# Performance work log

Hardware: AMD Instinct MI355X
Metric: run time of the kernel (lower is better)

## Reference

```python
import jax, jax.numpy as jnp
import numpy as np

B, T, E, H, D = 4, 2048, 1024, 16, 64


def setup_inputs() -> dict:
    key = jax.random.key(0)
    k1, k2, k3, k4 = jax.random.split(key, 4)
    s = 1.0 / np.sqrt(E)
    return {
        "x": jax.random.normal(k1, (B, T, E), dtype=jnp.float32),
        "wj_w": jax.random.uniform(k2, (E, E), jnp.float32, -s, s),   # torch Linear weight (out,in)
        "wjv_w": jax.random.uniform(k3, (E, E), jnp.float32, -s, s),
        "wo_w": jax.random.uniform(k4, (E, H * D), jnp.float32, -s, s),
    }


def reference(x, wj_w, wjv_w, wo_w):
    b, t, e = x.shape
    # echo = x @ wj_w.T ; eb = echo @ wj_w  (F.linear with transposed weight)
    eb = (x @ wj_w.T) @ wj_w
    sc = jnp.sum(x * eb, axis=-1) / jnp.sqrt(jnp.asarray(e, x.dtype))  # (B,T)
    # rank-1 outer-product scores with strict-upper causal mask
    ja = sc[:, :, None] * sc[:, None, :]                               # (B,T,T)
    causal = jnp.tril(jnp.ones((t, t), dtype=bool))
    ja = jnp.where(causal[None], ja, -jnp.inf)
    ja = jax.nn.softmax(ja, axis=-1)                                   # (B,T,T)
    # values per head; attention map shared across heads (broadcast, not materialized)
    val = (x @ wjv_w.T).reshape(b, t, H, D)                            # (B,T,H,D)
    out = jnp.einsum("bts,bshd->bthd", ja, val)                       # (B,T,H,D)
    return out.reshape(b, t, H * D) @ wo_w.T                           # (B,T,E)
```

## Files before the change

### kernel.cpp

```cpp
#include <hip/hip_runtime.h>
#include <math.h>

#define R_ROWS 8192
#define T_SEQ  2048
#define E_DIM  1024
#define KC     32

typedef __attribute__((ext_vector_type(8))) short short8;
typedef __attribute__((ext_vector_type(4))) float f32x4;

__device__ __forceinline__ ushort f2bf(float f) {
  uint u = __float_as_uint(f);
  u += 0x7FFFu + ((u >> 16) & 1u);
  return (ushort)(u >> 16);
}
__device__ __forceinline__ float bf2f(ushort h) {
  return __uint_as_float(((uint)h) << 16);
}


__global__ __launch_bounds__(256) void cvt_split_frag(
    const float* __restrict__ in, ushort* __restrict__ hi,
    ushort* __restrict__ lo, int n)
{
  int g = blockIdx.x * 256 + threadIdx.x;
  if (g >= n) return;
  const int l = g & 15, h = (g >> 4) & 3;
  const int pq = g >> 6;
  const int q = pq & (KC - 1), p = pq >> 5;
  const size_t src = (size_t)(p * 16 + l) * 1024 + q * 32 + h * 8;
  const float4 v0 = *(const float4*)&in[src];
  const float4 v1 = *(const float4*)&in[src + 4];
  ushort hh[8], ll[8];
  const float v[8] = {v0.x, v0.y, v0.z, v0.w, v1.x, v1.y, v1.z, v1.w};
#pragma unroll
  for (int e = 0; e < 8; ++e) {
    hh[e] = f2bf(v[e]);
    ll[e] = f2bf(v[e] - bf2f(hh[e]));
  }
  *(uint4*)&hi[(size_t)g * 8] = *(const uint4*)hh;
  *(uint4*)&lo[(size_t)g * 8] = *(const uint4*)ll;
}

__global__ __launch_bounds__(256) void cvt_bf16_frag(
    const float* __restrict__ in, ushort* __restrict__ out, int n)
{
  int g = blockIdx.x * 256 + threadIdx.x;
  if (g >= n) return;
  const int l = g & 15, h = (g >> 4) & 3;
  const int pq = g >> 6;
  const int q = pq & (KC - 1), p = pq >> 5;
  const size_t src = (size_t)(p * 16 + l) * 1024 + q * 32 + h * 8;
  const float4 v0 = *(const float4*)&in[src];
  const float4 v1 = *(const float4*)&in[src + 4];
  ushort hh[8];
  const float v[8] = {v0.x, v0.y, v0.z, v0.w, v1.x, v1.y, v1.z, v1.w};
#pragma unroll
  for (int e = 0; e < 8; ++e) hh[e] = f2bf(v[e]);
  *(uint4*)&out[(size_t)g * 8] = *(const uint4*)hh;
}

__global__ __launch_bounds__(256) void cvt_bf16(
    const float* __restrict__ in, ushort* __restrict__ out, int n4)
{
  int i = blockIdx.x * 256 + threadIdx.x;
  if (i >= n4) return;
  float4 v = ((const float4*)in)[i];
  ushort4 o;
  o.x = f2bf(v.x); o.y = f2bf(v.y); o.z = f2bf(v.z); o.w = f2bf(v.w);
  ((ushort4*)out)[i] = o;
}

struct Frags { short8 ah[4], al[4], bh[4], bl[4]; };

__global__ __launch_bounds__(256, 2) void gemm_sq_direct(
    const ushort* __restrict__ xh, const ushort* __restrict__ xl,
    const ushort* __restrict__ wh, const ushort* __restrict__ wl,
    float* __restrict__ sc_raw)
{
  const int tid = threadIdx.x;
  const int m0 = blockIdx.y * 128, n0 = blockIdx.x * 128;
  const int wave = tid >> 6, lane = tid & 63;
  const int l15 = lane & 15, lq = lane >> 4;
  const int wm = (wave & 1) * 64, wn = (wave >> 1) * 64;

  size_t aoff[4], boff[4];
#pragma unroll
  for (int i = 0; i < 4; ++i)
    aoff[i] = ((size_t)(((m0 + wm) >> 4) + i) * KC * 4 + lq) * 128 + l15 * 8;
#pragma unroll
  for (int j = 0; j < 4; ++j)
    boff[j] = ((size_t)(((n0 + wn) >> 4) + j) * KC * 4 + lq) * 128 + l15 * 8;

  f32x4 acc[4][4] = {};
  Frags f0, f1;

  auto load = [&](Frags& f, int q) {
    const size_t dq = (size_t)q * 512;
#pragma unroll
    for (int i = 0; i < 4; ++i) {
      f.ah[i] = *(const short8*)(xh + aoff[i] + dq);
      f.al[i] = *(const short8*)(xl + aoff[i] + dq);
    }
#pragma unroll
    for (int j = 0; j < 4; ++j) {
      f.bh[j] = *(const short8*)(wh + boff[j] + dq);
      f.bl[j] = *(const short8*)(wl + boff[j] + dq);
    }
  };
  auto step = [&](const Frags& f) {
#pragma unroll
    for (int i = 0; i < 4; ++i)
#pragma unroll
      for (int j = 0; j < 4; ++j) {
        acc[i][j] = __builtin_amdgcn_mfma_f32_16x16x32_bf16(f.ah[i], f.bh[j], acc[i][j], 0, 0, 0);
        acc[i][j] = __builtin_amdgcn_mfma_f32_16x16x32_bf16(f.ah[i], f.bl[j], acc[i][j], 0, 0, 0);
        acc[i][j] = __builtin_amdgcn_mfma_f32_16x16x32_bf16(f.al[i], f.bh[j], acc[i][j], 0, 0, 0);
      }
  };

  load(f0, 0);
#pragma unroll 1
  for (int q = 0; q < KC; q += 2) {
    load(f1, q + 1);
    step(f0);
    if (q + 2 < KC) load(f0, q + 2);
    step(f1);
  }

  __shared__ float red[128][33];
#pragma unroll
  for (int i = 0; i < 4; ++i)
#pragma unroll
    for (int r = 0; r < 4; ++r) {
      const int row = wm + i * 16 + lq * 4 + r;
      float s = 0.f;
#pragma unroll
      for (int j = 0; j < 4; ++j) s += acc[i][j][r] * acc[i][j][r];
      red[row][(l15 << 1) | (wave >> 1)] = s;
    }
  __syncthreads();
  if (tid < 128) {
    float s = 0.f;
#pragma unroll
    for (int c = 0; c < 32; ++c) s += red[tid][c];
    atomicAdd(&sc_raw[m0 + tid], s);
  }
}

__global__ __launch_bounds__(1024) void scan_max(
    const float* __restrict__ sc_raw, float* __restrict__ sc,
    float* __restrict__ pmax)
{
  const int b = blockIdx.x;
  __shared__ float b0[T_SEQ];
  __shared__ float b1[T_SEQ];
  const int tid = threadIdx.x;
  for (int i = tid; i < T_SEQ; i += 1024) {
    const float v = sc_raw[b*T_SEQ + i] * 0.03125f;
    b0[i] = v;
    sc[b*T_SEQ + i] = v;
  }
  __syncthreads();
  float* src = b0; float* dst = b1;
  for (int off = 1; off < T_SEQ; off <<= 1) {
    for (int i = tid; i < T_SEQ; i += 1024)
      dst[i] = (i >= off) ? fmaxf(src[i], src[i - off]) : src[i];
    __syncthreads();
    float* tmp = src; src = dst; dst = tmp;
  }
  for (int i = tid; i < T_SEQ; i += 1024) pmax[b*T_SEQ + i] = src[i];
}

template<bool OUT_BF16>
__global__ __launch_bounds__(256) void gemm_bf16_bfrag(
    const ushort* __restrict__ A, const ushort* __restrict__ Bf,
    void* __restrict__ Cout, int N, int K)
{
  __shared__ ushort As[128][40];
  const int tid = threadIdx.x;
  const int m0 = blockIdx.y * 128, n0 = blockIdx.x * 128;
  const int wave = tid >> 6, lane = tid & 63;
  const int l15 = lane & 15, lq = lane >> 4;
  const int wm = (wave & 1) * 64, wn = (wave >> 1) * 64;
  const int srow = tid >> 2, scol = (tid & 3) * 8;
  const int Kc = K >> 5;

  f32x4 acc[4][4] = {};
  const ushort* Ap = A + (size_t)(m0 + srow) * K + scol;
  size_t boff[4];
#pragma unroll
  for (int j = 0; j < 4; ++j)
    boff[j] = ((size_t)(((n0 + wn) >> 4) + j) * Kc * 4 + lq) * 128 + l15 * 8;

  for (int q = 0; q < Kc; ++q) {
    const uint4 a0 = *(const uint4*)(Ap + q * 32);
    const uint4 a1 = *(const uint4*)(Ap + (size_t)64 * K + q * 32);
    short8 bfr[4];
#pragma unroll
    for (int j = 0; j < 4; ++j)
      bfr[j] = *(const short8*)(Bf + boff[j] + (size_t)q * 512);
    __syncthreads();
    *(uint4*)&As[srow     ][scol] = a0;
    *(uint4*)&As[srow + 64][scol] = a1;
    __syncthreads();
    short8 af[4];
#pragma unroll
    for (int i = 0; i < 4; ++i)
      af[i] = *(const short8*)&As[wm + i*16 + l15][lq*8];
#pragma unroll
    for (int i = 0; i < 4; ++i)
#pragma unroll
      for (int j = 0; j < 4; ++j)
        acc[i][j] = __builtin_amdgcn_mfma_f32_16x16x32_bf16(af[i], bfr[j], acc[i][j], 0, 0, 0);
  }

#pragma unroll
  for (int i = 0; i < 4; ++i)
#pragma unroll
    for (int j = 0; j < 4; ++j) {
      const int mb = m0 + wm + i*16 + lq*4;
      const int nb = n0 + wn + j*16 + l15;
#pragma unroll
      for (int r = 0; r < 4; ++r) {
        if (OUT_BF16)
          ((ushort*)Cout)[(size_t)(mb + r) * N + nb] = f2bf(acc[i][j][r]);
        else
          ((float*)Cout)[(size_t)(mb + r) * N + nb] = acc[i][j][r];
      }
    }
}

__global__ __launch_bounds__(512) void attn_mfma(
    const ushort* __restrict__ valT, const float* __restrict__ sc,
    const float* __restrict__ pmax, ushort* __restrict__ attnN)
{
  __shared__ float scs_all[T_SEQ];
  __shared__ ushort p[2][128][72];
  __shared__ float zsh[128][4];
  __shared__ float zinv[128];

  const int b  = blockIdx.z;
  const int e0 = blockIdx.x * 128;
  const int tid = threadIdx.x;
  const int wave = tid >> 6, lane = tid & 63;
  const int l15 = lane & 15, lq = lane >> 4;
  const int wm = (wave & 1) * 64;
  const int wn = (wave >> 1) * 32;
  const int bT = b * T_SEQ;

  *(float4*)&scs_all[tid * 4] = *(const float4*)&sc[bT + tid * 4];
  __syncthreads();

  const int prow = tid >> 2;
  const int pc = (tid & 3) * 16;

#pragma unroll 1
  for (int ph = 0; ph < 2; ++ph) {
    const int ty = ph == 0 ? (15 - (int)blockIdx.y) : (int)blockIdx.y;
    const int t0 = ty * 128;
    const int nchunk = 2 * ty + 2;

    const int tglob = t0 + prow;
    const float st = sc[bT + tglob];
    const float pm = pmax[bT + tglob];

    f32x4 acc[4][2] = {};
    float zp = 0.f;

    auto pgen = [&](int c, int buf) -> float {
      const int s0 = c * 64;
      float sv[16];
#pragma unroll
      for (int q = 0; q < 4; ++q)
        *(float4*)&sv[q*4] = *(const float4*)&scs_all[s0 + pc + q*4];
      ushort tmp[16];
      float z = 0.f;
#pragma unroll
      for (int k = 0; k < 16; ++k) {
        const int sg = s0 + pc + k;
        float pe = 0.f;
        if (sg <= tglob) pe = __expf(st * (sv[k] - pm));
        const ushort h = f2bf(pe);
        tmp[k] = h;
        z += bf2f(h);
      }
      *(uint4*)&p[buf][prow][pc    ] = *(const uint4*)&tmp[0];
      *(uint4*)&p[buf][prow][pc + 8] = *(const uint4*)&tmp[8];
      return z;
    };

    auto loadB = [&](short8* dst, int c) {
#pragma unroll
      for (int j = 0; j < 2; ++j)
#pragma unroll
        for (int ksi = 0; ksi < 2; ++ksi)
          dst[j*2 + ksi] = *(const short8*)&valT[
              (size_t)(e0 + wn + j*16 + l15) * R_ROWS + bT + c*64 + ksi*32 + lq*8];
    };

    auto mstep = [&](int buf, const short8* bfr) {
#pragma unroll
      for (int ksi = 0; ksi < 2; ++ksi) {
        short8 af[4];
#pragma unroll
        for (int i = 0; i < 4; ++i)
          af[i] = *(const short8*)&p[buf][wm + i*16 + l15][ksi*32 + lq*8];
#pragma unroll
        for (int i = 0; i < 4; ++i)
#pragma unroll
          for (int j = 0; j < 2; ++j)
            acc[i][j] = __builtin_amdgcn_mfma_f32_16x16x32_bf16(
                af[i], bfr[j*2 + ksi], acc[i][j], 0, 0, 0);
      }
    };

    short8 bA[4], bB[4];
    zp += pgen(0, 0);
    loadB(bA, 0);
    __syncthreads();

#pragma unroll 1
    for (int c = 0; c < nchunk; ++c) {
      if ((c & 1) == 0) {
        if (c + 1 < nchunk) { loadB(bB, c + 1); zp += pgen(c + 1, 1); }
        mstep(0, bA);
      } else {
        if (c + 1 < nchunk) { loadB(bA, c + 1); zp += pgen(c + 1, 0); }
        mstep(1, bB);
      }
      __syncthreads();
    }

    zsh[prow][tid & 3] = zp;
    __syncthreads();
    if (tid < 128)
      zinv[tid] = 1.0f / (zsh[tid][0] + zsh[tid][1] + zsh[tid][2] + zsh[tid][3]);
    __syncthreads();

#pragma unroll
    for (int i = 0; i < 4; ++i)
#pragma unroll
      for (int j = 0; j < 2; ++j) {
        const int nb = e0 + wn + j*16 + l15;
#pragma unroll
        for (int r = 0; r < 4; ++r) {
          const int ml = wm + i*16 + lq*4 + r;
          const float v = acc[i][j][r] * zinv[ml];
          attnN[(size_t)(bT + t0 + ml) * E_DIM + nb] = f2bf(v);
        }
      }
    __syncthreads();
  }
}

extern "C" void kernel_launch(void* const* d_in, const int* in_sizes, int n_in,
                              void* d_out, int out_size, void* d_ws, size_t ws_size,
                              hipStream_t stream) {
  (void)in_sizes; (void)n_in; (void)out_size; (void)ws_size;
  const float* x   = (const float*)d_in[0];
  const float* wj  = (const float*)d_in[1];
  const float* wjv = (const float*)d_in[2];
  const float* wo  = (const float*)d_in[3];
  float* out = (float*)d_out;

  ushort* xh_f  = (ushort*)d_ws;
  ushort* xl_f  = xh_f  + (size_t)R_ROWS * E_DIM;
  ushort* wjh_f = xl_f  + (size_t)R_ROWS * E_DIM;
  ushort* wjl_f = wjh_f + (size_t)E_DIM * E_DIM;
  ushort* wjvb  = wjl_f + (size_t)E_DIM * E_DIM;
  ushort* wob_f = wjvb  + (size_t)E_DIM * E_DIM;
  float* sc_raw = (float*)(wob_f + (size_t)E_DIM * E_DIM);
  float* sc     = sc_raw + R_ROWS;
  float* pmax   = sc + R_ROWS;
  ushort* valT  = xl_f;
  ushort* attnN = xh_f;

  hipMemsetAsync(sc_raw, 0, R_ROWS * sizeof(float), stream);

  cvt_split_frag<<<R_ROWS*E_DIM/8/256, 256, 0, stream>>>(x,  xh_f,  xl_f,  R_ROWS*E_DIM/8);
  cvt_split_frag<<<E_DIM*E_DIM/8/256, 256, 0, stream>>>(wj, wjh_f, wjl_f, E_DIM*E_DIM/8);
  cvt_bf16<<<E_DIM*E_DIM/4/256, 256, 0, stream>>>(wjv, wjvb, E_DIM*E_DIM/4);
  cvt_bf16_frag<<<E_DIM*E_DIM/8/256, 256, 0, stream>>>(wo, wob_f, E_DIM*E_DIM/8);

  gemm_sq_direct<<<dim3(E_DIM/128, R_ROWS/128), 256, 0, stream>>>(
      xh_f, xl_f, wjh_f, wjl_f, sc_raw);
  scan_max<<<4, 1024, 0, stream>>>(sc_raw, sc, pmax);

  gemm_bf16_bfrag<true><<<dim3(R_ROWS/128, E_DIM/128), 256, 0, stream>>>(
      wjvb, xh_f, valT, R_ROWS, E_DIM);

  attn_mfma<<<dim3(E_DIM/128, 8, 4), 512, 0, stream>>>(valT, sc, pmax, attnN);

  gemm_bf16_bfrag<false><<<dim3(E_DIM/128, R_ROWS/128), 256, 0, stream>>>(
      attnN, wob_f, out, E_DIM, E_DIM);
}
```

Before: 271.8 us.

## Split attention into P-generation kernel and fragment-layout MFMA GEMM

The causal softmax probability tiles are now computed once per batch in a separate kernel and stored to workspace in MFMA fragment order, with row sums accumulated atomically into a Z buffer. The attention GEMM reads P fragments and values straight from global memory into registers with double buffering and no LDS or barriers, and uses a 64x64 per-wave tile. Previously each of the 8 column blocks recomputed the exponentials. The cost is an extra launch, global traffic for the P tiles, and a reworked workspace layout that reuses the wj buffers once they are consumed.

```diff
diff --git a/kernel.cpp b/kernel.cpp
--- a/kernel.cpp
+++ b/kernel.cpp
@@ -172,6 +172,142 @@
   for (int i = tid; i < T_SEQ; i += 1024) pmax[b*T_SEQ + i] = src[i];
 }
 
+__global__ __launch_bounds__(256) void pgen(
+    const float* __restrict__ sc, const float* __restrict__ pmax,
+    ushort* __restrict__ Pfrag, float* __restrict__ Z)
+{
+  const int b = blockIdx.y;
+  const int cb = blockIdx.x;
+  int ty = (int)((sqrtf(4.0f * cb + 1.0f) - 1.0f) * 0.5f);
+  while ((ty + 1) * (ty + 2) <= cb) ++ty;
+  while (ty * (ty + 1) > cb) --ty;
+  const int c = cb - ty * (ty + 1);
+  const int t0 = ty * 128, s0 = c * 64;
+  const int bT = b * T_SEQ;
+  const int tid = threadIdx.x;
+
+  __shared__ float stv[128], pmv[128], scs[64], zacc[128];
+  if (tid < 128) {
+    stv[tid] = sc[bT + t0 + tid];
+    pmv[tid] = pmax[bT + t0 + tid];
+    zacc[tid] = 0.f;
+  } else if (tid < 192) {
+    scs[tid - 128] = sc[bT + s0 + (tid - 128)];
+  }
+  __syncthreads();
+
+  ushort* base = Pfrag + (size_t)(b * 272 + cb) * 8192;
+#pragma unroll
+  for (int i = 0; i < 4; ++i) {
+    const int run = tid * 4 + i;
+    const int r  = ((run >> 7) << 4) | (run & 15);
+    const int sb = (((run >> 6) & 1) << 5) | (((run >> 4) & 3) << 3);
+    const float st = stv[r], pm = pmv[r];
+    const int tg = t0 + r, sg0 = s0 + sb;
+    ushort tmp[8];
+    float z = 0.f;
+#pragma unroll
+    for (int k = 0; k < 8; ++k) {
+      float pe = 0.f;
+      if (sg0 + k <= tg) pe = __expf(st * (scs[sb + k] - pm));
+      const ushort hb = f2bf(pe);
+      tmp[k] = hb;
+      z += bf2f(hb);
+    }
+    *(uint4*)(base + run * 8) = *(const uint4*)tmp;
+    if (z != 0.f) atomicAdd(&zacc[r], z);
+  }
+  __syncthreads();
+  if (tid < 128 && zacc[tid] != 0.f)
+    atomicAdd(&Z[bT + t0 + tid], zacc[tid]);
+}
+
+__global__ __launch_bounds__(256, 2) void attn_gemm(
+    const ushort* __restrict__ Pfrag, const ushort* __restrict__ valT,
+    const float* __restrict__ Z, ushort* __restrict__ attnN)
+{
+  const int b = blockIdx.z;
+  const int e0 = blockIdx.x * 128;
+  const int tid = threadIdx.x;
+  const int wave = tid >> 6, lane = tid & 63;
+  const int l15 = lane & 15, lq = lane >> 4;
+  const int wm = (wave & 1) * 64, wn = (wave >> 1) * 64;
+  const int bT = b * T_SEQ;
+
+#pragma unroll 1
+  for (int ph = 0; ph < 2; ++ph) {
+    const int ty = ph ? (int)blockIdx.y : 15 - (int)blockIdx.y;
+    const int t0 = ty * 128;
+    const int nch = 2 * ty + 2;
+    const ushort* pb = Pfrag + (size_t)(b * 272 + ty * (ty + 1)) * 8192;
+
+    size_t aoffs[4][2];
+#pragma unroll
+    for (int i = 0; i < 4; ++i)
+#pragma unroll
+      for (int ksi = 0; ksi < 2; ++ksi)
+        aoffs[i][ksi] =
+            (size_t)(((((wm >> 4) + i) * 2 + ksi) * 4 + lq) * 128 + l15 * 8);
+    const ushort* vbase = valT + bT + lq * 8;
+    size_t voffs[4];
+#pragma unroll
+    for (int j = 0; j < 4; ++j)
+      voffs[j] = (size_t)(e0 + wn + j * 16 + l15) * R_ROWS;
+
+    f32x4 acc[4][4] = {};
+    short8 a0[4][2], v0[4][2], a1[4][2], v1[4][2];
+
+    auto load = [&](short8 (&a)[4][2], short8 (&v)[4][2], int c) {
+      const ushort* cbp = pb + (size_t)c * 8192;
+      const ushort* vb = vbase + c * 64;
+#pragma unroll
+      for (int i = 0; i < 4; ++i) {
+        a[i][0] = *(const short8*)(cbp + aoffs[i][0]);
+        a[i][1] = *(const short8*)(cbp + aoffs[i][1]);
+      }
+#pragma unroll
+      for (int j = 0; j < 4; ++j) {
+        v[j][0] = *(const short8*)(vb + voffs[j]);
+        v[j][1] = *(const short8*)(vb + voffs[j] + 32);
+      }
+    };
+    auto step = [&](short8 (&a)[4][2], short8 (&v)[4][2]) {
+#pragma unroll
+      for (int ksi = 0; ksi < 2; ++ksi)
+#pragma unroll
+        for (int i = 0; i < 4; ++i)
+#pragma unroll
+          for (int j = 0; j < 4; ++j)
+            acc[i][j] = __builtin_amdgcn_mfma_f32_16x16x32_bf16(
+                a[i][ksi], v[j][ksi], acc[i][j], 0, 0, 0);
+    };
+
+    load(a0, v0, 0);
+#pragma unroll 1
+    for (int c = 0; c < nch; c += 2) {
+      load(a1, v1, c + 1);
+      step(a0, v0);
+      if (c + 2 < nch) load(a0, v0, c + 2);
+      step(a1, v1);
+    }
+
+#pragma unroll
+    for (int i = 0; i < 4; ++i) {
+      const int mlb = t0 + wm + i * 16 + lq * 4;
+      float zi[4];
+#pragma unroll
+      for (int r = 0; r < 4; ++r) zi[r] = 1.0f / Z[bT + mlb + r];
+#pragma unroll
+      for (int j = 0; j < 4; ++j) {
+        const int nb = e0 + wn + j * 16 + l15;
+#pragma unroll
+        for (int r = 0; r < 4; ++r)
+          attnN[(size_t)(bT + mlb + r) * E_DIM + nb] = f2bf(acc[i][j][r] * zi[r]);
+      }
+    }
+  }
+}
+
 template<bool OUT_BF16>
 __global__ __launch_bounds__(256) void gemm_bf16_bfrag(
     const ushort* __restrict__ A, const ushort* __restrict__ Bf,
@@ -229,129 +365,6 @@
           ((float*)Cout)[(size_t)(mb + r) * N + nb] = acc[i][j][r];
       }
     }
-}
-
-__global__ __launch_bounds__(512) void attn_mfma(
-    const ushort* __restrict__ valT, const float* __restrict__ sc,
-    const float* __restrict__ pmax, ushort* __restrict__ attnN)
-{
-  __shared__ float scs_all[T_SEQ];
-  __shared__ ushort p[2][128][72];
-  __shared__ float zsh[128][4];
-  __shared__ float zinv[128];
-
-  const int b  = blockIdx.z;
-  const int e0 = blockIdx.x * 128;
-  const int tid = threadIdx.x;
-  const int wave = tid >> 6, lane = tid & 63;
-  const int l15 = lane & 15, lq = lane >> 4;
-  const int wm = (wave & 1) * 64;
-  const int wn = (wave >> 1) * 32;
-  const int bT = b * T_SEQ;
-
-  *(float4*)&scs_all[tid * 4] = *(const float4*)&sc[bT + tid * 4];
-  __syncthreads();
-
-  const int prow = tid >> 2;
-  const int pc = (tid & 3) * 16;
-
-#pragma unroll 1
-  for (int ph = 0; ph < 2; ++ph) {
-    const int ty = ph == 0 ? (15 - (int)blockIdx.y) : (int)blockIdx.y;
-    const int t0 = ty * 128;
-    const int nchunk = 2 * ty + 2;
-
-    const int tglob = t0 + prow;
-    const float st = sc[bT + tglob];
-    const float pm = pmax[bT + tglob];
-
-    f32x4 acc[4][2] = {};
-    float zp = 0.f;
-
-    auto pgen = [&](int c, int buf) -> float {
-      const int s0 = c * 64;
-      float sv[16];
-#pragma unroll
-      for (int q = 0; q < 4; ++q)
-        *(float4*)&sv[q*4] = *(const float4*)&scs_all[s0 + pc + q*4];
-      ushort tmp[16];
-      float z = 0.f;
-#pragma unroll
-      for (int k = 0; k < 16; ++k) {
-        const int sg = s0 + pc + k;
-        float pe = 0.f;
-        if (sg <= tglob) pe = __expf(st * (sv[k] - pm));
-        const ushort h = f2bf(pe);
-        tmp[k] = h;
-        z += bf2f(h);
-      }
-      *(uint4*)&p[buf][prow][pc    ] = *(const uint4*)&tmp[0];
-      *(uint4*)&p[buf][prow][pc + 8] = *(const uint4*)&tmp[8];
-      return z;
-    };
-
-    auto loadB = [&](short8* dst, int c) {
-#pragma unroll
-      for (int j = 0; j < 2; ++j)
-#pragma unroll
-        for (int ksi = 0; ksi < 2; ++ksi)
-          dst[j*2 + ksi] = *(const short8*)&valT[
-              (size_t)(e0 + wn + j*16 + l15) * R_ROWS + bT + c*64 + ksi*32 + lq*8];
-    };
-
-    auto mstep = [&](int buf, const short8* bfr) {
-#pragma unroll
-      for (int ksi = 0; ksi < 2; ++ksi) {
-        short8 af[4];
-#pragma unroll
-        for (int i = 0; i < 4; ++i)
-          af[i] = *(const short8*)&p[buf][wm + i*16 + l15][ksi*32 + lq*8];
-#pragma unroll
-        for (int i = 0; i < 4; ++i)
-#pragma unroll
-          for (int j = 0; j < 2; ++j)
-            acc[i][j] = __builtin_amdgcn_mfma_f32_16x16x32_bf16(
-                af[i], bfr[j*2 + ksi], acc[i][j], 0, 0, 0);
-      }
-    };
-
-    short8 bA[4], bB[4];
-    zp += pgen(0, 0);
-    loadB(bA, 0);
-    __syncthreads();
-
-#pragma unroll 1
-    for (int c = 0; c < nchunk; ++c) {
-      if ((c & 1) == 0) {
-        if (c + 1 < nchunk) { loadB(bB, c + 1); zp += pgen(c + 1, 1); }
-        mstep(0, bA);
-      } else {
-        if (c + 1 < nchunk) { loadB(bA, c + 1); zp += pgen(c + 1, 0); }
-        mstep(1, bB);
-      }
-      __syncthreads();
-    }
-
-    zsh[prow][tid & 3] = zp;
-    __syncthreads();
-    if (tid < 128)
-      zinv[tid] = 1.0f / (zsh[tid][0] + zsh[tid][1] + zsh[tid][2] + zsh[tid][3]);
-    __syncthreads();
-
-#pragma unroll
-    for (int i = 0; i < 4; ++i)
-#pragma unroll
-      for (int j = 0; j < 2; ++j) {
-        const int nb = e0 + wn + j*16 + l15;
-#pragma unroll
-        for (int r = 0; r < 4; ++r) {
-          const int ml = wm + i*16 + lq*4 + r;
-          const float v = acc[i][j][r] * zinv[ml];
-          attnN[(size_t)(bT + t0 + ml) * E_DIM + nb] = f2bf(v);
-        }
-      }
-    __syncthreads();
-  }
 }
 
 extern "C" void kernel_launch(void* const* d_in, const int* in_sizes, int n_in,
@@ -368,15 +381,17 @@
   ushort* xl_f  = xh_f  + (size_t)R_ROWS * E_DIM;
   ushort* wjh_f = xl_f  + (size_t)R_ROWS * E_DIM;
   ushort* wjl_f = wjh_f + (size_t)E_DIM * E_DIM;
-  ushort* wjvb  = wjl_f + (size_t)E_DIM * E_DIM;
-  ushort* wob_f = wjvb  + (size_t)E_DIM * E_DIM;
-  float* sc_raw = (float*)(wob_f + (size_t)E_DIM * E_DIM);
-  float* sc     = sc_raw + R_ROWS;
+  ushort* Pfrag = wjh_f;
+  float* sc_raw = (float*)(Pfrag + (size_t)1088 * 8192);
+  float* Zbuf   = sc_raw + R_ROWS;
+  float* sc     = Zbuf + R_ROWS;
   float* pmax   = sc + R_ROWS;
+  ushort* wjvb  = (ushort*)(pmax + R_ROWS);
+  ushort* wob_f = wjvb + (size_t)E_DIM * E_DIM;
   ushort* valT  = xl_f;
   ushort* attnN = xh_f;
 
-  hipMemsetAsync(sc_raw, 0, R_ROWS * sizeof(float), stream);
+  hipMemsetAsync(sc_raw, 0, 2 * R_ROWS * sizeof(float), stream);
 
   cvt_split_frag<<<R_ROWS*E_DIM/8/256, 256, 0, stream>>>(x,  xh_f,  xl_f,  R_ROWS*E_DIM/8);
   cvt_split_frag<<<E_DIM*E_DIM/8/256, 256, 0, stream>>>(wj, wjh_f, wjl_f, E_DIM*E_DIM/8);
@@ -390,7 +405,9 @@
   gemm_bf16_bfrag<true><<<dim3(R_ROWS/128, E_DIM/128), 256, 0, stream>>>(
       wjvb, xh_f, valT, R_ROWS, E_DIM);
 
-  attn_mfma<<<dim3(E_DIM/128, 8, 4), 512, 0, stream>>>(valT, sc, pmax, attnN);
+  pgen<<<dim3(272, 4), 256, 0, stream>>>(sc, pmax, Pfrag, Zbuf);
+
+  attn_gemm<<<dim3(E_DIM/128, 8, 4), 256, 0, stream>>>(Pfrag, valT, Zbuf, attnN);
 
   gemm_bf16_bfrag<false><<<dim3(E_DIM/128, R_ROWS/128), 256, 0, stream>>>(
       attnN, wob_f, out, E_DIM, E_DIM);
```

After: 291.6 us. +7.3%, slower.

## Retile attention kernel to 64 query rows by 256 value columns with finer causal chunks

Applied to the files above, without the earlier changes.

Changes the attention tile from 128 query rows by 128 value columns to 64 rows by 256 columns, with each wave computing 32x64 instead of 64x32. Causal chunking now skips at 64-row granularity, which cuts the wasted masked work along the diagonal. The mask check is applied only on the last chunk, and the exponent argument is folded into a single fmaf. The cost is more B-fragment registers per wave and more blocks, while P generation per value column is amortized over twice as many columns.

```diff
diff --git a/kernel.cpp b/kernel.cpp
--- a/kernel.cpp
+++ b/kernel.cpp
@@ -236,63 +236,71 @@
     const float* __restrict__ pmax, ushort* __restrict__ attnN)
 {
   __shared__ float scs_all[T_SEQ];
-  __shared__ ushort p[2][128][72];
-  __shared__ float zsh[128][4];
-  __shared__ float zinv[128];
+  __shared__ ushort p[2][64][72];
+  __shared__ float zsh[64][9];
+  __shared__ float zinv[64];
 
   const int b  = blockIdx.z;
-  const int e0 = blockIdx.x * 128;
+  const int e0 = blockIdx.x * 256;
   const int tid = threadIdx.x;
   const int wave = tid >> 6, lane = tid & 63;
   const int l15 = lane & 15, lq = lane >> 4;
-  const int wm = (wave & 1) * 64;
-  const int wn = (wave >> 1) * 32;
+  const int wm = (wave & 1) * 32;
+  const int wn = (wave >> 1) * 64;
   const int bT = b * T_SEQ;
 
   *(float4*)&scs_all[tid * 4] = *(const float4*)&sc[bT + tid * 4];
   __syncthreads();
 
-  const int prow = tid >> 2;
-  const int pc = (tid & 3) * 16;
+  const int prow = tid >> 3;
+  const int pc = (tid & 7) * 8;
 
 #pragma unroll 1
   for (int ph = 0; ph < 2; ++ph) {
-    const int ty = ph == 0 ? (15 - (int)blockIdx.y) : (int)blockIdx.y;
-    const int t0 = ty * 128;
-    const int nchunk = 2 * ty + 2;
-
+    const int ty = ph ? (int)blockIdx.y : 31 - (int)blockIdx.y;
+    const int t0 = ty * 64;
+    const int nch = ty + 1;
+
+    const float st = scs_all[t0 + prow];
+    const float nd = -st * pmax[bT + t0 + prow];
     const int tglob = t0 + prow;
-    const float st = sc[bT + tglob];
-    const float pm = pmax[bT + tglob];
-
-    f32x4 acc[4][2] = {};
+
+    f32x4 acc[2][4] = {};
     float zp = 0.f;
 
     auto pgen = [&](int c, int buf) -> float {
       const int s0 = c * 64;
-      float sv[16];
-#pragma unroll
-      for (int q = 0; q < 4; ++q)
-        *(float4*)&sv[q*4] = *(const float4*)&scs_all[s0 + pc + q*4];
-      ushort tmp[16];
+      float sv[8];
+      *(float4*)&sv[0] = *(const float4*)&scs_all[s0 + pc];
+      *(float4*)&sv[4] = *(const float4*)&scs_all[s0 + pc + 4];
+      ushort tmp[8];
       float z = 0.f;
-#pragma unroll
-      for (int k = 0; k < 16; ++k) {
-        const int sg = s0 + pc + k;
-        float pe = 0.f;
-        if (sg <= tglob) pe = __expf(st * (sv[k] - pm));
-        const ushort h = f2bf(pe);
-        tmp[k] = h;
-        z += bf2f(h);
-      }
-      *(uint4*)&p[buf][prow][pc    ] = *(const uint4*)&tmp[0];
-      *(uint4*)&p[buf][prow][pc + 8] = *(const uint4*)&tmp[8];
+      if (c < nch - 1) {
+#pragma unroll
+        for (int k = 0; k < 8; ++k) {
+          const float pe = __expf(fmaf(st, sv[k], nd));
+          const ushort h = f2bf(pe);
+          tmp[k] = h;
+          z += bf2f(h);
+        }
+      } else {
+        const int sg0 = s0 + pc;
+#pragma unroll
+        for (int k = 0; k < 8; ++k) {
+          float pe = 0.f;
+          if (sg0 + k <= tglob) pe = __expf(fmaf(st, sv[k], nd));
+          const ushort h = f2bf(pe);
+          tmp[k] = h;
+          z += bf2f(h);
+        }
+      }
+      *(uint4*)&p[buf][prow][pc] = *(const uint4*)tmp;
       return z;
     };
 
     auto loadB = [&](short8* dst, int c) {
 #pragma unroll
-      for (int j = 0; j < 2; ++j)
+      for (int j = 0; j < 4; ++j)
 #pragma unroll
         for (int ksi = 0; ksi < 2; ++ksi)
           dst[j*2 + ksi] = *(const short8*)&valT[
@@ -302,46 +310,50 @@
     auto mstep = [&](int buf, const short8* bfr) {
 #pragma unroll
       for (int ksi = 0; ksi < 2; ++ksi) {
-        short8 af[4];
-#pragma unroll
-        for (int i = 0; i < 4; ++i)
+        short8 af[2];
+#pragma unroll
+        for (int i = 0; i < 2; ++i)
           af[i] = *(const short8*)&p[buf][wm + i*16 + l15][ksi*32 + lq*8];
 #pragma unroll
-        for (int i = 0; i < 4; ++i)
-#pragma unroll
-          for (int j = 0; j < 2; ++j)
+        for (int i = 0; i < 2; ++i)
+#pragma unroll
+          for (int j = 0; j < 4; ++j)
             acc[i][j] = __builtin_amdgcn_mfma_f32_16x16x32_bf16(
                 af[i], bfr[j*2 + ksi], acc[i][j], 0, 0, 0);
       }
     };
 
-    short8 bA[4], bB[4];
+    short8 bA[8], bB[8];
     zp += pgen(0, 0);
     loadB(bA, 0);
     __syncthreads();
 
 #pragma unroll 1
-    for (int c = 0; c < nchunk; ++c) {
+    for (int c = 0; c < nch; ++c) {
       if ((c & 1) == 0) {
-        if (c + 1 < nchunk) { loadB(bB, c + 1); zp += pgen(c + 1, 1); }
+        if (c + 1 < nch) { loadB(bB, c + 1); zp += pgen(c + 1, 1); }
         mstep(0, bA);
       } else {
-        if (c + 1 < nchunk) { loadB(bA, c + 1); zp += pgen(c + 1, 0); }
+        if (c + 1 < nch) { loadB(bA, c + 1); zp += pgen(c + 1, 0); }
         mstep(1, bB);
       }
       __syncthreads();
     }
 
-    zsh[prow][tid & 3] = zp;
-    __syncthreads();
-    if (tid < 128)
-      zinv[tid] = 1.0f / (zsh[tid][0] + zsh[tid][1] + zsh[tid][2] + zsh[tid][3]);
-    __syncthreads();
-
-#pragma unroll
-    for (int i = 0; i < 4; ++i)
-#pragma unroll
-      for (int j = 0; j < 2; ++j) {
+    zsh[prow][tid & 7] = zp;
+    __syncthreads();
+    if (tid < 64) {
+      float z = 0.f;
+#pragma unroll
+      for (int q = 0; q < 8; ++q) z += zsh[tid][q];
+      zinv[tid] = 1.0f / z;
+    }
+    __syncthreads();
+
+#pragma unroll
+    for (int i = 0; i < 2; ++i)
+#pragma unroll
+      for (int j = 0; j < 4; ++j) {
         const int nb = e0 + wn + j*16 + l15;
 #pragma unroll
         for (int r = 0; r < 4; ++r) {
@@ -390,7 +402,7 @@
   gemm_bf16_bfrag<true><<<dim3(R_ROWS/128, E_DIM/128), 256, 0, stream>>>(
       wjvb, xh_f, valT, R_ROWS, E_DIM);
 
-  attn_mfma<<<dim3(E_DIM/128, 8, 4), 512, 0, stream>>>(valT, sc, pmax, attnN);
+  attn_mfma<<<dim3(E_DIM/256, 16, 4), 512, 0, stream>>>(valT, sc, pmax, attnN);
 
   gemm_bf16_bfrag<false><<<dim3(E_DIM/128, R_ROWS/128), 256, 0, stream>>>(
       attnN, wob_f, out, E_DIM, E_DIM);
```

Result: slower. 283.9 us (+4.5%).

## Emit value GEMM in MFMA fragment layout and split attention tiles per block

Applied to the files above, without the earlier changes.

The value-projection GEMM now stages its output through shared memory and writes it in the MFMA B-fragment order. The attention kernel can then load B operands with contiguous 16-byte reads instead of strided ones. The attention grid doubles so each block handles one query tile instead of a balanced pair. Unmasked chunks also skip the causal compare and use a single fma before the exp. The cost is extra LDS traffic and a sync in the GEMM epilogue, and the per-block work becomes imbalanced across the grid.

```diff
diff --git a/kernel.cpp b/kernel.cpp
--- a/kernel.cpp
+++ b/kernel.cpp
@@ -172,10 +172,71 @@
   for (int i = tid; i < T_SEQ; i += 1024) pmax[b*T_SEQ + i] = src[i];
 }
 
-template<bool OUT_BF16>
-__global__ __launch_bounds__(256) void gemm_bf16_bfrag(
+__global__ __launch_bounds__(256) void gemm_val_frag(
     const ushort* __restrict__ A, const ushort* __restrict__ Bf,
-    void* __restrict__ Cout, int N, int K)
+    ushort* __restrict__ valTf, int K)
+{
+  __shared__ ushort As[128][40];
+  __shared__ ushort Et[4][64][72];
+  const int tid = threadIdx.x;
+  const int m0 = blockIdx.y * 128, n0 = blockIdx.x * 128;
+  const int wave = tid >> 6, lane = tid & 63;
+  const int l15 = lane & 15, lq = lane >> 4;
+  const int wm = (wave & 1) * 64, wn = (wave >> 1) * 64;
+  const int srow = tid >> 2, scol = (tid & 3) * 8;
+  const int Kc = K >> 5;
+
+  f32x4 acc[4][4] = {};
+  const ushort* Ap = A + (size_t)(m0 + srow) * K + scol;
+  size_t boff[4];
+#pragma unroll
+  for (int j = 0; j < 4; ++j)
+    boff[j] = ((size_t)(((n0 + wn) >> 4) + j) * Kc * 4 + lq) * 128 + l15 * 8;
+
+  for (int q = 0; q < Kc; ++q) {
+    const uint4 a0 = *(const uint4*)(Ap + q * 32);
+    const uint4 a1 = *(const uint4*)(Ap + (size_t)64 * K + q * 32);
+    short8 bfr[4];
+#pragma unroll
+    for (int j = 0; j < 4; ++j)
+      bfr[j] = *(const short8*)(Bf + boff[j] + (size_t)q * 512);
+    __syncthreads();
+    *(uint4*)&As[srow     ][scol] = a0;
+    *(uint4*)&As[srow + 64][scol] = a1;
+    __syncthreads();
+    short8 af[4];
+#pragma unroll
+    for (int i = 0; i < 4; ++i)
+      af[i] = *(const short8*)&As[wm + i*16 + l15][lq*8];
+#pragma unroll
+    for (int i = 0; i < 4; ++i)
+#pragma unroll
+      for (int j = 0; j < 4; ++j)
+        acc[i][j] = __builtin_amdgcn_mfma_f32_16x16x32_bf16(af[i], bfr[j], acc[i][j], 0, 0, 0);
+  }
+
+#pragma unroll
+  for (int i = 0; i < 4; ++i)
+#pragma unroll
+    for (int j = 0; j < 4; ++j)
+#pragma unroll
+      for (int r = 0; r < 4; ++r)
+        Et[wave][i*16 + lq*4 + r][j*16 + l15] = f2bf(acc[i][j][r]);
+
+  const int pe0 = (m0 + wm) >> 4;
+  const int qk0 = (n0 + wn) >> 5;
+#pragma unroll
+  for (int i2 = 0; i2 < 4; ++i2)
+#pragma unroll
+    for (int ks = 0; ks < 2; ++ks) {
+      uint4 w = *(const uint4*)&Et[wave][i2*16 + l15][ks*32 + lq*8];
+      *(uint4*)&valTf[(size_t)(((pe0 + i2) * 256 + qk0 + ks) * 4 + lq) * 128 + l15*8] = w;
+    }
+}
+
+__global__ __launch_bounds__(256) void gemm_out_bfrag(
+    const ushort* __restrict__ A, const ushort* __restrict__ Bf,
+    float* __restrict__ Cout, int N, int K)
 {
   __shared__ ushort As[128][40];
   const int tid = threadIdx.x;
@@ -222,17 +283,13 @@
       const int mb = m0 + wm + i*16 + lq*4;
       const int nb = n0 + wn + j*16 + l15;
 #pragma unroll
-      for (int r = 0; r < 4; ++r) {
-        if (OUT_BF16)
-          ((ushort*)Cout)[(size_t)(mb + r) * N + nb] = f2bf(acc[i][j][r]);
-        else
-          ((float*)Cout)[(size_t)(mb + r) * N + nb] = acc[i][j][r];
-      }
+      for (int r = 0; r < 4; ++r)
+        Cout[(size_t)(mb + r) * N + nb] = acc[i][j][r];
     }
 }
 
 __global__ __launch_bounds__(512) void attn_mfma(
-    const ushort* __restrict__ valT, const float* __restrict__ sc,
+    const ushort* __restrict__ valTf, const float* __restrict__ sc,
     const float* __restrict__ pmax, ushort* __restrict__ attnN)
 {
   __shared__ float scs_all[T_SEQ];
@@ -242,6 +299,9 @@
 
   const int b  = blockIdx.z;
   const int e0 = blockIdx.x * 128;
+  const int ty = 15 - (int)blockIdx.y;
+  const int t0 = ty * 128;
+  const int nch = 2 * ty + 2;
   const int tid = threadIdx.x;
   const int wave = tid >> 6, lane = tid & 63;
   const int l15 = lane & 15, lq = lane >> 4;
@@ -254,104 +314,110 @@
 
   const int prow = tid >> 2;
   const int pc = (tid & 3) * 16;
-
-#pragma unroll 1
-  for (int ph = 0; ph < 2; ++ph) {
-    const int ty = ph == 0 ? (15 - (int)blockIdx.y) : (int)blockIdx.y;
-    const int t0 = ty * 128;
-    const int nchunk = 2 * ty + 2;
-
-    const int tglob = t0 + prow;
-    const float st = sc[bT + tglob];
-    const float pm = pmax[bT + tglob];
-
-    f32x4 acc[4][2] = {};
-    float zp = 0.f;
-
-    auto pgen = [&](int c, int buf) -> float {
-      const int s0 = c * 64;
-      float sv[16];
-#pragma unroll
-      for (int q = 0; q < 4; ++q)
-        *(float4*)&sv[q*4] = *(const float4*)&scs_all[s0 + pc + q*4];
-      ushort tmp[16];
-      float z = 0.f;
+  const int tglob = t0 + prow;
+  const float st = scs_all[tglob];
+  const float nd = -st * pmax[bT + tglob];
+
+  f32x4 acc[4][2] = {};
+  float zp = 0.f;
+
+  auto pgen = [&](int c, int buf) -> float {
+    const int s0 = c * 64;
+    float sv[16];
+#pragma unroll
+    for (int q = 0; q < 4; ++q)
+      *(float4*)&sv[q*4] = *(const float4*)&scs_all[s0 + pc + 4*q];
+    ushort tmp[16];
+    float z = 0.f;
+    if (c < nch - 2) {
 #pragma unroll
       for (int k = 0; k < 16; ++k) {
-        const int sg = s0 + pc + k;
-        float pe = 0.f;
-        if (sg <= tglob) pe = __expf(st * (sv[k] - pm));
+        const float pe = __expf(fmaf(st, sv[k], nd));
         const ushort h = f2bf(pe);
         tmp[k] = h;
         z += bf2f(h);
       }
-      *(uint4*)&p[buf][prow][pc    ] = *(const uint4*)&tmp[0];
-      *(uint4*)&p[buf][prow][pc + 8] = *(const uint4*)&tmp[8];
-      return z;
-    };
-
-    auto loadB = [&](short8* dst, int c) {
-#pragma unroll
-      for (int j = 0; j < 2; ++j)
-#pragma unroll
-        for (int ksi = 0; ksi < 2; ++ksi)
-          dst[j*2 + ksi] = *(const short8*)&valT[
-              (size_t)(e0 + wn + j*16 + l15) * R_ROWS + bT + c*64 + ksi*32 + lq*8];
-    };
-
-    auto mstep = [&](int buf, const short8* bfr) {
-#pragma unroll
-      for (int ksi = 0; ksi < 2; ++ksi) {
-        short8 af[4];
-#pragma unroll
-        for (int i = 0; i < 4; ++i)
-          af[i] = *(const short8*)&p[buf][wm + i*16 + l15][ksi*32 + lq*8];
-#pragma unroll
-        for (int i = 0; i < 4; ++i)
-#pragma unroll
-          for (int j = 0; j < 2; ++j)
-            acc[i][j] = __builtin_amdgcn_mfma_f32_16x16x32_bf16(
-                af[i], bfr[j*2 + ksi], acc[i][j], 0, 0, 0);
+    } else {
+      const int sg0 = s0 + pc;
+#pragma unroll
+      for (int k = 0; k < 16; ++k) {
+        float pe = 0.f;
+        if (sg0 + k <= tglob) pe = __expf(fmaf(st, sv[k], nd));
+        const ushort h = f2bf(pe);
+        tmp[k] = h;
+        z += bf2f(h);
       }
-    };
-
-    short8 bA[4], bB[4];
-    zp += pgen(0, 0);
-    loadB(bA, 0);
-    __syncthreads();
+    }
+    *(uint4*)&p[buf][prow][pc    ] = *(const uint4*)&tmp[0];
+    *(uint4*)&p[buf][prow][pc + 8] = *(const uint4*)&tmp[8];
+    return z;
+  };
+
+  size_t vo[2];
+#pragma unroll
+  for (int j = 0; j < 2; ++j)
+    vo[j] = (size_t)(((e0 + wn) >> 4) + j) * 256;
+  auto loadB = [&](short8* dst, int c) {
+    const int qk = b * 64 + c * 2;
+#pragma unroll
+    for (int j = 0; j < 2; ++j)
+#pragma unroll
+      for (int ksi = 0; ksi < 2; ++ksi)
+        dst[j*2 + ksi] = *(const short8*)&valTf[
+            ((vo[j] + qk + ksi) * 4 + lq) * 128 + l15 * 8];
+  };
+
+  auto mstep = [&](int buf, const short8* bfr) {
+#pragma unroll
+    for (int ksi = 0; ksi < 2; ++ksi) {
+      short8 af[4];
+#pragma unroll
+      for (int i = 0; i < 4; ++i)
+        af[i] = *(const short8*)&p[buf][wm + i*16 + l15][ksi*32 + lq*8];
+#pragma unroll
+      for (int i = 0; i < 4; ++i)
+#pragma unroll
+        for (int j = 0; j < 2; ++j)
+          acc[i][j] = __builtin_amdgcn_mfma_f32_16x16x32_bf16(
+              af[i], bfr[j*2 + ksi], acc[i][j], 0, 0, 0);
+    }
+  };
+
+  short8 bA[4], bB[4];
+  zp += pgen(0, 0);
+  loadB(bA, 0);
+  __syncthreads();
 
 #pragma unroll 1
-    for (int c = 0; c < nchunk; ++c) {
-      if ((c & 1) == 0) {
-        if (c + 1 < nchunk) { loadB(bB, c + 1); zp += pgen(c + 1, 1); }
-        mstep(0, bA);
-      } else {
-        if (c + 1 < nchunk) { loadB(bA, c + 1); zp += pgen(c + 1, 0); }
-        mstep(1, bB);
+  for (int c = 0; c < nch; ++c) {
+    if ((c & 1) == 0) {
+      if (c + 1 < nch) { loadB(bB, c + 1); zp += pgen(c + 1, 1); }
+      mstep(0, bA);
+    } else {
+      if (c + 1 < nch) { loadB(bA, c + 1); zp += pgen(c + 1, 0); }
+      mstep(1, bB);
+    }
+    __syncthreads();
+  }
+
+  zsh[prow][tid & 3] = zp;
+  __syncthreads();
+  if (tid < 128)
+    zinv[tid] = 1.0f / (zsh[tid][0] + zsh[tid][1] + zsh[tid][2] + zsh[tid][3]);
+  __syncthreads();
+
+#pragma unroll
+  for (int i = 0; i < 4; ++i)
+#pragma unroll
+    for (int j = 0; j < 2; ++j) {
+      const int nb = e0 + wn + j*16 + l15;
+#pragma unroll
+      for (int r = 0; r < 4; ++r) {
+        const int ml = wm + i*16 + lq*4 + r;
+        const float v = acc[i][j][r] * zinv[ml];
+        attnN[(size_t)(bT + t0 + ml) * E_DIM + nb] = f2bf(v);
       }
-      __syncthreads();
-    }
-
-    zsh[prow][tid & 3] = zp;
-    __syncthreads();
-    if (tid < 128)
-      zinv[tid] = 1.0f / (zsh[tid][0] + zsh[tid][1] + zsh[tid][2] + zsh[tid][3]);
-    __syncthreads();
-
-#pragma unroll
-    for (int i = 0; i < 4; ++i)
-#pragma unroll
-      for (int j = 0; j < 2; ++j) {
-        const int nb = e0 + wn + j*16 + l15;
-#pragma unroll
-        for (int r = 0; r < 4; ++r) {
-          const int ml = wm + i*16 + lq*4 + r;
-          const float v = acc[i][j][r] * zinv[ml];
-          attnN[(size_t)(bT + t0 + ml) * E_DIM + nb] = f2bf(v);
-        }
-      }
-    __syncthreads();
-  }
+    }
 }
 
 extern "C" void kernel_launch(void* const* d_in, const int* in_sizes, int n_in,
@@ -373,7 +439,7 @@
   float* sc_raw = (float*)(wob_f + (size_t)E_DIM * E_DIM);
   float* sc     = sc_raw + R_ROWS;
   float* pmax   = sc + R_ROWS;
-  ushort* valT  = xl_f;
+  ushort* valTf = xl_f;
   ushort* attnN = xh_f;
 
   hipMemsetAsync(sc_raw, 0, R_ROWS * sizeof(float), stream);
@@ -387,11 +453,11 @@
       xh_f, xl_f, wjh_f, wjl_f, sc_raw);
   scan_max<<<4, 1024, 0, stream>>>(sc_raw, sc, pmax);
 
-  gemm_bf16_bfrag<true><<<dim3(R_ROWS/128, E_DIM/128), 256, 0, stream>>>(
-      wjvb, xh_f, valT, R_ROWS, E_DIM);
-
-  attn_mfma<<<dim3(E_DIM/128, 8, 4), 512, 0, stream>>>(valT, sc, pmax, attnN);
-
-  gemm_bf16_bfrag<false><<<dim3(E_DIM/128, R_ROWS/128), 256, 0, stream>>>(
+  gemm_val_frag<<<dim3(R_ROWS/128, E_DIM/128), 256, 0, stream>>>(
+      wjvb, xh_f, valTf, E_DIM);
+
+  attn_mfma<<<dim3(E_DIM/128, 16, 4), 512, 0, stream>>>(valTf, sc, pmax, attnN);
+
+  gemm_out_bfrag<<<dim3(E_DIM/128, R_ROWS/128), 256, 0, stream>>>(
       attnN, wob_f, out, E_DIM, E_DIM);
 }
```

New measurement: 284.7 us. 4.8% more time.
